# Performance work log

Hardware: AMD Instinct MI355X
Metric: run time of the kernel (lower is better)

## Reference

```python
import jax, jax.numpy as jnp
import numpy as np

NUM_HEADS = 8


def setup_inputs() -> dict:
    key = jax.random.key(0)
    ks = jax.random.split(key, 7)
    B, H, W, C = 1, 64, 64, 512
    x = jax.random.normal(ks[0], (B, H, W, C), dtype=jnp.float32)
    # lat in [-pi/2, pi/2), lon in [0, 2*pi) radians
    lat_grid = (jax.random.uniform(ks[1], (H, W), dtype=jnp.float32) - 0.5) * np.float32(np.pi)
    lon_grid = jax.random.uniform(ks[2], (H, W), dtype=jnp.float32) * np.float32(2 * np.pi)
    w_qkv = jax.random.normal(ks[3], (3 * C, C), dtype=jnp.float32) * 0.02
    b_qkv = jax.random.normal(ks[4], (3 * C,), dtype=jnp.float32) * 0.02
    w_out = jax.random.normal(ks[5], (C, C), dtype=jnp.float32) * 0.02
    b_out = jax.random.normal(ks[6], (C,), dtype=jnp.float32) * 0.02
    return {"x": x, "lat_grid": lat_grid, "lon_grid": lon_grid,
            "w_qkv": w_qkv, "b_qkv": b_qkv, "w_out": w_out, "b_out": b_out}


def _distance_bias(lat_grid, lon_grid):
    # Haversine great-circle distance between all pairs of grid points.
    lat = lat_grid.reshape(-1)  # [N]
    lon = lon_grid.reshape(-1)
    dlat = lat[None, :] - lat[:, None]  # [N, N]
    dlon = lon[None, :] - lon[:, None]
    a = jnp.sin(dlat / 2) ** 2 + jnp.cos(lat)[:, None] * jnp.cos(lat)[None, :] * jnp.sin(dlon / 2) ** 2
    dist = 2.0 * jnp.arcsin(jnp.sqrt(jnp.clip(a, 0.0, 1.0)))
    # torch .std() is unbiased (ddof=1)
    return -dist / jnp.std(dist, ddof=1)


def reference(x, lat_grid, lon_grid, w_qkv, b_qkv, w_out, b_out):
    B, H, W, C = x.shape
    nh = NUM_HEADS
    dh = C // nh
    N = H * W
    qkv = x @ w_qkv.T + b_qkv  # [B, H, W, 3C]
    qkv = qkv.reshape(B, N, 3, nh, dh)
    q = jnp.transpose(qkv[:, :, 0], (0, 2, 1, 3))  # [B, nh, N, dh]
    k = jnp.transpose(qkv[:, :, 1], (0, 2, 1, 3))
    v = jnp.transpose(qkv[:, :, 2], (0, 2, 1, 3))
    scale = np.float32(1.0 / np.sqrt(dh))
    attn = jnp.einsum("bhnd,bhmd->bhnm", q, k) * scale  # [B, nh, N, N]
    attn = attn + _distance_bias(lat_grid, lon_grid)[None, None]
    attn = jax.nn.softmax(attn, axis=-1)  # dropout is identity in eval
    out = jnp.einsum("bhnm,bhmd->bhnd", attn, v)  # [B, nh, N, dh]
    out = jnp.transpose(out, (0, 2, 1, 3)).reshape(B, H, W, C)
    return out @ w_out.T + b_out
```

## Files before the change

### kernel.cpp

```cpp
#include <hip/hip_runtime.h>
#include <hip/hip_bf16.h>


typedef __attribute__((ext_vector_type(8))) short bf16x8;
typedef __attribute__((ext_vector_type(4))) float f32x4;

#define MFMA16(a, b, c) __builtin_amdgcn_mfma_f32_16x16x32_bf16(a, b, c, 0, 0, 0)

__device__ __forceinline__ unsigned short f2b(float f) {
    union { float f; unsigned int i; } v;
    v.f = f;
    unsigned int lsb = (v.i >> 16) & 1u;
    unsigned int r = v.i + 0x7fffu + lsb;
    return (unsigned short)(r >> 16);
}

__global__ __launch_bounds__(256) void prep_kernel(
    const float* __restrict__ lat, const float* __restrict__ lon,
    float* __restrict__ dist, double* __restrict__ partials,
    const float* __restrict__ x, unsigned short* __restrict__ xb,
    const float* __restrict__ wq, unsigned short* __restrict__ wqb,
    const float* __restrict__ wo, unsigned short* __restrict__ wob) {
    __shared__ float sl_i[64], sc_i[64], so_i[64];
    __shared__ float sl_j[64], sc_j[64], so_j[64];
    __shared__ float dstage[64][65];
    __shared__ double rs[256], rs2[256];

    int b = blockIdx.x;
    int tid = threadIdx.x;

    if (b < 2080) {
        int ti = 0, rem = b;
        while (rem >= 64 - ti) { rem -= 64 - ti; ti++; }
        int tj = ti + rem;
        int i0 = ti << 6, j0 = tj << 6;

        if (tid < 64) {
            float la = lat[i0 + tid];
            sl_i[tid] = la; sc_i[tid] = __cosf(la); so_i[tid] = lon[i0 + tid];
        } else if (tid < 128) {
            int t = tid - 64;
            float la = lat[j0 + t];
            sl_j[t] = la; sc_j[t] = __cosf(la); so_j[t] = lon[j0 + t];
        }
        __syncthreads();

        float s = 0.f, s2 = 0.f;
        int col = tid & 63;
        int w = tid >> 6;
        int pcol = ((col & 15) << 2) + (col >> 4);
        float latj = sl_j[col], cj = sc_j[col], lonj = so_j[col];
#pragma unroll
        for (int kk = 0; kk < 16; kk++) {
            int row = (kk << 2) + w;
            float dlat = latj - sl_i[row];
            float dlon = lonj - so_i[row];
            float h1 = __sinf(0.5f * dlat);
            float h2 = __sinf(0.5f * dlon);
            float a = h1 * h1 + sc_i[row] * cj * h2 * h2;
            a = fminf(fmaxf(a, 0.0f), 1.0f);
            float d = 2.0f * asinf(sqrtf(a));
            dist[(size_t)(i0 + row) * 4096 + j0 + pcol] = d;
            dstage[row][col] = d;
            s += d;
            s2 += d * d;
        }
        if (ti != tj) {
            __syncthreads();
#pragma unroll
            for (int kk = 0; kk < 16; kk++) {
                int row2 = (kk << 2) + w;
                float dt = dstage[col][row2];
                dist[(size_t)(j0 + row2) * 4096 + i0 + pcol] = dt;
            }
            s *= 2.f; s2 *= 2.f;
        }
        rs[tid] = (double)s; rs2[tid] = (double)s2;
        __syncthreads();
        for (int off = 128; off > 0; off >>= 1) {
            if (tid < off) { rs[tid] += rs[tid + off]; rs2[tid] += rs2[tid + off]; }
            __syncthreads();
        }
        if (tid == 0) {
            partials[2 * b] = rs[0];
            partials[2 * b + 1] = rs2[0];
        }
        return;
    }

    const float* in; unsigned short* out; int t;
    if (b < 3104)      { in = x;  out = xb;  t = (b - 2080) * 256 + tid; }
    else if (b < 3488) { in = wq; out = wqb; t = (b - 3104) * 256 + tid; }
    else               { in = wo; out = wob; t = (b - 3488) * 256 + tid; }
    int l = t & 15, qd = (t >> 4) & 3, c = (t >> 6) & 15, g = t >> 10;
    const float* src = in + ((size_t)g * 16 + l) * 512 + c * 32 + qd * 8;
    float4 v0 = *(const float4*)src;
    float4 v1 = *(const float4*)(src + 4);
    ushort4 u0, u1;
    u0.x = f2b(v0.x); u0.y = f2b(v0.y); u0.z = f2b(v0.z); u0.w = f2b(v0.w);
    u1.x = f2b(v1.x); u1.y = f2b(v1.y); u1.z = f2b(v1.z); u1.w = f2b(v1.w);
    unsigned short* dst = out + (size_t)t * 8;
    *(ushort4*)dst = u0;
    *(ushort4*)(dst + 4) = u1;
}

__global__ __launch_bounds__(256) void qkv_gemm(
    const unsigned short* __restrict__ x, const unsigned short* __restrict__ w,
    const float* __restrict__ b,
    unsigned short* __restrict__ q, unsigned short* __restrict__ k,
    unsigned short* __restrict__ vt,
    const double* __restrict__ partials, float* __restrict__ neg_inv_std) {
    __shared__ unsigned short stage[64][72];
    __shared__ double rs[256], rs2[256];
    int lane = threadIdx.x & 63, wave = threadIdx.x >> 6;
    int l16 = lane & 15, quad = lane >> 4;

    if (blockIdx.x == 24) {
        if (blockIdx.y != 0) return;
        int tid = threadIdx.x;
        double s = 0.0, s2 = 0.0;
        for (int i = tid; i < 2080; i += 256) {
            s += partials[2 * i];
            s2 += partials[2 * i + 1];
        }
        rs[tid] = s; rs2[tid] = s2;
        __syncthreads();
        for (int off = 128; off > 0; off >>= 1) {
            if (tid < off) { rs[tid] += rs[tid + off]; rs2[tid] += rs2[tid + off]; }
            __syncthreads();
        }
        if (tid == 0) {
            double n = 16777216.0;
            double mean = rs[0] / n;
            double var = (rs2[0] - n * mean * mean) / (n - 1.0);
            *neg_inv_std = (float)(-1.0 / sqrt(var));
        }
        return;
    }

    int m0 = blockIdx.y * 64 + wave * 16;
    int n0 = blockIdx.x * 64;

    const unsigned short* abase = x + (size_t)(blockIdx.y * 4 + wave) * 8192 + lane * 8;
    f32x4 acc[4];
#pragma unroll
    for (int nb = 0; nb < 4; nb++) acc[nb] = (f32x4){0.f, 0.f, 0.f, 0.f};

    for (int k0 = 0; k0 < 512; k0 += 32) {
        bf16x8 af = *(const bf16x8*)(abase + (k0 >> 5) * 512);
#pragma unroll
        for (int nb = 0; nb < 4; nb++) {
            bf16x8 bf = *(const bf16x8*)(w + (size_t)((n0 >> 4) + nb) * 8192
                                           + (k0 >> 5) * 512 + lane * 8);
            acc[nb] = MFMA16(af, bf, acc[nb]);
        }
    }
    if (blockIdx.x < 8) {
#pragma unroll
        for (int nb = 0; nb < 4; nb++) {
            int j = n0 + nb * 16 + l16;
            float bj = b[j];
            int h = j >> 6, d = j & 63;
#pragma unroll
            for (int r = 0; r < 4; r++) {
                int n = m0 + quad * 4 + r;
                q[((size_t)h * 4096 + n) * 64 + d] = f2b((acc[nb][r] + bj) * 0.125f);
            }
        }
    } else if (blockIdx.x < 16) {
        int h = blockIdx.x - 8;
#pragma unroll
        for (int nb = 0; nb < 4; nb++) {
            int d = nb * 16 + l16;
            float bj = b[512 + h * 64 + d];
#pragma unroll
            for (int r = 0; r < 4; r++)
                stage[wave * 16 + quad * 4 + r][d] = f2b(acc[nb][r] + bj);
        }
        __syncthreads();
        unsigned short* kb = k + ((size_t)h << 18) + (size_t)blockIdx.y * 4096;
#pragma unroll
        for (int p = 0; p < 2; p++) {
            int rid = p * 256 + threadIdx.x;
            int t = rid >> 7;
            int rem = rid & 127;
            int half = rem >> 6, qd = (rem >> 4) & 3, l = rem & 15;
            const unsigned short* src = &stage[t * 16 + l][half * 32 + qd * 8];
            unsigned short* dst = kb + t * 1024 + half * 512 + qd * 128 + l * 8;
            *(uint4*)dst = *(const uint4*)src;
        }
    } else {
        int h = blockIdx.x - 16;
#pragma unroll
        for (int nb = 0; nb < 4; nb++) {
            int d = nb * 16 + l16;
            float bj = b[1024 + h * 64 + d];
#pragma unroll
            for (int r = 0; r < 4; r++)
                stage[d][quad * 16 + r * 4 + wave] = f2b(acc[nb][r] + bj);
        }
        __syncthreads();
        int t = threadIdx.x;
        int d = t >> 2;
        int nq = (t & 3) * 16;
        unsigned short* dst = vt + ((size_t)h << 18) + (size_t)blockIdx.y * 4096
                            + (d >> 4) * 1024 + ((nq >> 5) & 1) * 512
                            + ((nq >> 3) & 3) * 128 + (d & 15) * 8;
        const unsigned short* src = &stage[d][nq];
        *(uint4*)dst = *(const uint4*)src;
        *(uint4*)(dst + 128) = *(const uint4*)(src + 8);
    }
}

__device__ __forceinline__ void attn_step(
    const unsigned short* __restrict__ kptr, const unsigned short* __restrict__ vtp,
    short* __restrict__ pb, int h, int kv0, int lane, int l16, int quad,
    bf16x8 qf0, bf16x8 qf1, float4 (&dv)[4], const float* __restrict__ drow,
    int kv_next, float nis, f32x4 (&o)[4], float (&lam)[4]) {
    size_t tbase = ((size_t)h << 18) + ((size_t)kv0 << 6) + lane * 8;
    const unsigned short* kb = kptr + tbase;
    const unsigned short* vb = vtp + tbase;
    f32x4 s[4];
    __builtin_amdgcn_s_setprio(1);
#pragma unroll
    for (int cb = 0; cb < 4; cb++) {
        bf16x8 kf0 = *(const bf16x8*)(kb + cb * 1024);
        bf16x8 kf1 = *(const bf16x8*)(kb + cb * 1024 + 512);
        f32x4 z = (f32x4){0.f, 0.f, 0.f, 0.f};
        z = MFMA16(qf0, kf0, z);
        z = MFMA16(qf1, kf1, z);
        s[cb] = z;
    }
    __builtin_amdgcn_s_setprio(0);
    bf16x8 vf[8];
#pragma unroll
    for (int db = 0; db < 4; db++) {
        vf[2 * db]     = *(const bf16x8*)(vb + db * 1024);
        vf[2 * db + 1] = *(const bf16x8*)(vb + db * 1024 + 512);
    }
#pragma unroll
    for (int r = 0; r < 4; r++) {
        s[0][r] = fmaf(dv[r].x, nis, s[0][r]);
        s[1][r] = fmaf(dv[r].y, nis, s[1][r]);
        s[2][r] = fmaf(dv[r].z, nis, s[2][r]);
        s[3][r] = fmaf(dv[r].w, nis, s[3][r]);
    }
#pragma unroll
    for (int r = 0; r < 4; r++)
        dv[r] = *(const float4*)(drow + (size_t)r * 4096 + kv_next);
#pragma unroll
    for (int r = 0; r < 4; r++) {
        float p0 = __expf(s[0][r]);
        float p1 = __expf(s[1][r]);
        float p2 = __expf(s[2][r]);
        float p3 = __expf(s[3][r]);
        lam[r] += (p0 + p1) + (p2 + p3);
        unsigned int w0 = (unsigned int)f2b(p0) | ((unsigned int)f2b(p1) << 16);
        unsigned int w1 = (unsigned int)f2b(p2) | ((unsigned int)f2b(p3) << 16);
        uint2 pk; pk.x = w0; pk.y = w1;
        *(uint2*)(pb + (quad * 4 + r) * 72 + l16 * 4) = pk;
    }
    bf16x8 pf0 = *(const bf16x8*)(pb + l16 * 72 + quad * 8);
    bf16x8 pf1 = *(const bf16x8*)(pb + l16 * 72 + 32 + quad * 8);
    __builtin_amdgcn_s_setprio(1);
#pragma unroll
    for (int db = 0; db < 4; db++) {
        o[db] = MFMA16(pf0, vf[2 * db], o[db]);
        o[db] = MFMA16(pf1, vf[2 * db + 1], o[db]);
    }
    __builtin_amdgcn_s_setprio(0);
}

__global__ __launch_bounds__(512, 4) void attn_kernel(
    const unsigned short* __restrict__ q, const unsigned short* __restrict__ k,
    const unsigned short* __restrict__ vt, const float* __restrict__ dist,
    const float* __restrict__ nis_p, unsigned short* __restrict__ att) {
    __shared__ __align__(16) char smem[18432];
    int tid = threadIdx.x;
    int lane = tid & 63, wave = tid >> 6;
    int l16 = lane & 15, quad = lane >> 4;
    int b = blockIdx.x;
    int xcd = b & 7, j = b >> 3;
    int h  = (xcd & 3) * 2 + (j & 1);
    int qs = (xcd >> 2) * 64 + (j >> 1);
    int qgl = wave & 1;
    int qt = wave >> 1;
    int q0 = qs * 32 + qgl * 16;
    int kvbase = qt * 1024;
    float nis = *nis_p;

    short* pb = (short*)smem + wave * 1152;

    const unsigned short* qbase = q + ((size_t)h * 4096 + q0 + l16) * 64 + quad * 8;
    bf16x8 qf0 = *(const bf16x8*)(qbase);
    bf16x8 qf1 = *(const bf16x8*)(qbase + 32);

    f32x4 o[4];
    float lam[4];
#pragma unroll
    for (int r = 0; r < 4; r++) {
        lam[r] = 0.f;
        o[0][r] = 0.f; o[1][r] = 0.f; o[2][r] = 0.f; o[3][r] = 0.f;
    }

    const float* drow = dist + (size_t)(q0 + quad * 4) * 4096 + l16 * 4;
    float4 dv[4];
#pragma unroll
    for (int r = 0; r < 4; r++)
        dv[r] = *(const float4*)(drow + (size_t)r * 4096 + kvbase);

    for (int it = 0; it < 16; ++it) {
        int kv0 = kvbase + it * 64;
        int kvn = (it == 15) ? kvbase : kv0 + 64;
        attn_step(k, vt, pb, h, kv0, lane, l16, quad, qf0, qf1, dv, drow, kvn,
                  nis, o, lam);
    }

#pragma unroll
    for (int r = 0; r < 4; r++)
#pragma unroll
        for (int off = 1; off < 16; off <<= 1)
            lam[r] += __shfl_xor(lam[r], off, 64);

    __syncthreads();
    float* obuf = (float*)smem;
    float* lbuf = (float*)(smem + 8192);
    if (l16 == 0)
#pragma unroll
        for (int r = 0; r < 4; r++)
            lbuf[qt * 32 + qgl * 16 + quad * 4 + r] = lam[r];
    if (qt == 0) {
#pragma unroll
        for (int db = 0; db < 4; db++)
#pragma unroll
            for (int r = 0; r < 4; r++)
                obuf[(qgl * 16 + quad * 4 + r) * 64 + db * 16 + l16] = o[db][r];
    }
    __syncthreads();
    if (qt == 1) {
#pragma unroll
        for (int db = 0; db < 4; db++)
#pragma unroll
            for (int r = 0; r < 4; r++)
                obuf[(qgl * 16 + quad * 4 + r) * 64 + db * 16 + l16] += o[db][r];
    }
    __syncthreads();
    if (qt == 2) {
#pragma unroll
        for (int db = 0; db < 4; db++)
#pragma unroll
            for (int r = 0; r < 4; r++)
                obuf[(qgl * 16 + quad * 4 + r) * 64 + db * 16 + l16] += o[db][r];
    }
    __syncthreads();
    if (qt == 3) {
#pragma unroll
        for (int db = 0; db < 4; db++)
#pragma unroll
            for (int r = 0; r < 4; r++)
                obuf[(qgl * 16 + quad * 4 + r) * 64 + db * 16 + l16] += o[db][r];
    }
    __syncthreads();

    int rl = tid >> 4;
    int d4 = (tid & 15) * 4;
    float L = lbuf[rl] + lbuf[32 + rl] + lbuf[64 + rl] + lbuf[96 + rl];
    float rinv = 1.0f / L;
    const float* ob = obuf + rl * 64 + d4;
    ushort4 ua;
    ua.x = f2b(ob[0] * rinv); ua.y = f2b(ob[1] * rinv);
    ua.z = f2b(ob[2] * rinv); ua.w = f2b(ob[3] * rinv);
    int row = qs * 32 + rl;
    int col = h * 64 + d4;
    size_t dst = (size_t)(row >> 4) * 8192 + (col >> 5) * 512
               + ((col >> 3) & 3) * 128 + (row & 15) * 8 + (col & 7);
    *(ushort4*)(att + dst) = ua;
}

__global__ __launch_bounds__(256) void out_gemm(
    const unsigned short* __restrict__ att, const unsigned short* __restrict__ w,
    const float* __restrict__ b, float* __restrict__ out) {
    int lane = threadIdx.x & 63, wave = threadIdx.x >> 6;
    int l16 = lane & 15, quad = lane >> 4;
    int m0 = blockIdx.y * 64 + wave * 16;
    int n0 = blockIdx.x * 64;

    const unsigned short* abase = att + (size_t)(blockIdx.y * 4 + wave) * 8192 + lane * 8;
    f32x4 acc[4];
#pragma unroll
    for (int nb = 0; nb < 4; nb++) acc[nb] = (f32x4){0.f, 0.f, 0.f, 0.f};

    for (int k0 = 0; k0 < 512; k0 += 32) {
        bf16x8 af = *(const bf16x8*)(abase + (k0 >> 5) * 512);
#pragma unroll
        for (int nb = 0; nb < 4; nb++) {
            bf16x8 bf = *(const bf16x8*)(w + (size_t)((n0 >> 4) + nb) * 8192
                                           + (k0 >> 5) * 512 + lane * 8);
            acc[nb] = MFMA16(af, bf, acc[nb]);
        }
    }
#pragma unroll
    for (int nb = 0; nb < 4; nb++) {
        float bj = b[n0 + nb * 16 + l16];
#pragma unroll
        for (int r = 0; r < 4; r++)
            out[(size_t)(m0 + quad * 4 + r) * 512 + n0 + nb * 16 + l16] =
                acc[nb][r] + bj;
    }
}

extern "C" void kernel_launch(void* const* d_in, const int* in_sizes, int n_in,
                              void* d_out, int out_size, void* d_ws, size_t ws_size,
                              hipStream_t stream) {
    const float* x    = (const float*)d_in[0];
    const float* lat  = (const float*)d_in[1];
    const float* lon  = (const float*)d_in[2];
    const float* wqkv = (const float*)d_in[3];
    const float* bqkv = (const float*)d_in[4];
    const float* wout = (const float*)d_in[5];
    const float* bout = (const float*)d_in[6];
    float* out = (float*)d_out;

    char* ws = (char*)d_ws;
    float* dist        = (float*)ws;
    double* partials   = (double*)(ws + 67108864);
    float* nis         = (float*)(ws + 67108864 + 65536);
    unsigned short* q  = (unsigned short*)(ws + 67108864 + 65600);
    unsigned short* k  = q  + (size_t)8 * 4096 * 64;
    unsigned short* vt = k  + (size_t)8 * 4096 * 64;
    unsigned short* att = vt + (size_t)8 * 4096 * 64;
    unsigned short* xb  = att + (size_t)4096 * 512;
    unsigned short* wqb = xb  + (size_t)4096 * 512;
    unsigned short* wob = wqb + (size_t)1536 * 512;

    prep_kernel<<<3616, 256, 0, stream>>>(lat, lon, dist, partials,
                                          x, xb, wqkv, wqb, wout, wob);
    qkv_gemm<<<dim3(25, 64), 256, 0, stream>>>(xb, wqb, bqkv, q, k, vt,
                                               partials, nis);
    attn_kernel<<<1024, 512, 0, stream>>>(q, k, vt, dist, nis, att);
    out_gemm<<<dim3(8, 64), 256, 0, stream>>>(att, wob, bout, out);
}
```

Measured before the change: 212.9 us.

## Software-pipeline attention loop by computing next tile's QK scores early

```diff
diff --git a/kernel.cpp b/kernel.cpp
--- a/kernel.cpp
+++ b/kernel.cpp
@@ -210,65 +210,6 @@
         *(uint4*)dst = *(const uint4*)src;
         *(uint4*)(dst + 128) = *(const uint4*)(src + 8);
     }
-}
-
-__device__ __forceinline__ void attn_step(
-    const unsigned short* __restrict__ kptr, const unsigned short* __restrict__ vtp,
-    short* __restrict__ pb, int h, int kv0, int lane, int l16, int quad,
-    bf16x8 qf0, bf16x8 qf1, float4 (&dv)[4], const float* __restrict__ drow,
-    int kv_next, float nis, f32x4 (&o)[4], float (&lam)[4]) {
-    size_t tbase = ((size_t)h << 18) + ((size_t)kv0 << 6) + lane * 8;
-    const unsigned short* kb = kptr + tbase;
-    const unsigned short* vb = vtp + tbase;
-    f32x4 s[4];
-    __builtin_amdgcn_s_setprio(1);
-#pragma unroll
-    for (int cb = 0; cb < 4; cb++) {
-        bf16x8 kf0 = *(const bf16x8*)(kb + cb * 1024);
-        bf16x8 kf1 = *(const bf16x8*)(kb + cb * 1024 + 512);
-        f32x4 z = (f32x4){0.f, 0.f, 0.f, 0.f};
-        z = MFMA16(qf0, kf0, z);
-        z = MFMA16(qf1, kf1, z);
-        s[cb] = z;
-    }
-    __builtin_amdgcn_s_setprio(0);
-    bf16x8 vf[8];
-#pragma unroll
-    for (int db = 0; db < 4; db++) {
-        vf[2 * db]     = *(const bf16x8*)(vb + db * 1024);
-        vf[2 * db + 1] = *(const bf16x8*)(vb + db * 1024 + 512);
-    }
-#pragma unroll
-    for (int r = 0; r < 4; r++) {
-        s[0][r] = fmaf(dv[r].x, nis, s[0][r]);
-        s[1][r] = fmaf(dv[r].y, nis, s[1][r]);
-        s[2][r] = fmaf(dv[r].z, nis, s[2][r]);
-        s[3][r] = fmaf(dv[r].w, nis, s[3][r]);
-    }
-#pragma unroll
-    for (int r = 0; r < 4; r++)
-        dv[r] = *(const float4*)(drow + (size_t)r * 4096 + kv_next);
-#pragma unroll
-    for (int r = 0; r < 4; r++) {
-        float p0 = __expf(s[0][r]);
-        float p1 = __expf(s[1][r]);
-        float p2 = __expf(s[2][r]);
-        float p3 = __expf(s[3][r]);
-        lam[r] += (p0 + p1) + (p2 + p3);
-        unsigned int w0 = (unsigned int)f2b(p0) | ((unsigned int)f2b(p1) << 16);
-        unsigned int w1 = (unsigned int)f2b(p2) | ((unsigned int)f2b(p3) << 16);
-        uint2 pk; pk.x = w0; pk.y = w1;
-        *(uint2*)(pb + (quad * 4 + r) * 72 + l16 * 4) = pk;
-    }
-    bf16x8 pf0 = *(const bf16x8*)(pb + l16 * 72 + quad * 8);
-    bf16x8 pf1 = *(const bf16x8*)(pb + l16 * 72 + 32 + quad * 8);
-    __builtin_amdgcn_s_setprio(1);
-#pragma unroll
-    for (int db = 0; db < 4; db++) {
-        o[db] = MFMA16(pf0, vf[2 * db], o[db]);
-        o[db] = MFMA16(pf1, vf[2 * db + 1], o[db]);
-    }
-    __builtin_amdgcn_s_setprio(0);
 }
 
 __global__ __launch_bounds__(512, 4) void attn_kernel(
@@ -295,6 +236,8 @@
     bf16x8 qf0 = *(const bf16x8*)(qbase);
     bf16x8 qf1 = *(const bf16x8*)(qbase + 32);
 
+    size_t hbase = ((size_t)h << 18) + (size_t)lane * 8;
+
     f32x4 o[4];
     float lam[4];
 #pragma unroll
@@ -309,11 +252,80 @@
     for (int r = 0; r < 4; r++)
         dv[r] = *(const float4*)(drow + (size_t)r * 4096 + kvbase);
 
+    f32x4 s[4];
+    {
+        const unsigned short* kb = k + hbase + ((size_t)kvbase << 6);
+        __builtin_amdgcn_s_setprio(1);
+#pragma unroll
+        for (int cb = 0; cb < 4; cb++) {
+            bf16x8 kf0 = *(const bf16x8*)(kb + cb * 1024);
+            bf16x8 kf1 = *(const bf16x8*)(kb + cb * 1024 + 512);
+            f32x4 z = (f32x4){0.f, 0.f, 0.f, 0.f};
+            z = MFMA16(qf0, kf0, z);
+            z = MFMA16(qf1, kf1, z);
+            s[cb] = z;
+        }
+        __builtin_amdgcn_s_setprio(0);
+    }
+
     for (int it = 0; it < 16; ++it) {
         int kv0 = kvbase + it * 64;
         int kvn = (it == 15) ? kvbase : kv0 + 64;
-        attn_step(k, vt, pb, h, kv0, lane, l16, quad, qf0, qf1, dv, drow, kvn,
-                  nis, o, lam);
+#pragma unroll
+        for (int r = 0; r < 4; r++) {
+            s[0][r] = fmaf(dv[r].x, nis, s[0][r]);
+            s[1][r] = fmaf(dv[r].y, nis, s[1][r]);
+            s[2][r] = fmaf(dv[r].z, nis, s[2][r]);
+            s[3][r] = fmaf(dv[r].w, nis, s[3][r]);
+        }
+#pragma unroll
+        for (int r = 0; r < 4; r++)
+            dv[r] = *(const float4*)(drow + (size_t)r * 4096 + kvn);
+#pragma unroll
+        for (int r = 0; r < 4; r++) {
+            float p0 = __expf(s[0][r]);
+            float p1 = __expf(s[1][r]);
+            float p2 = __expf(s[2][r]);
+            float p3 = __expf(s[3][r]);
+            lam[r] += (p0 + p1) + (p2 + p3);
+            unsigned int w0 = (unsigned int)f2b(p0) | ((unsigned int)f2b(p1) << 16);
+            unsigned int w1 = (unsigned int)f2b(p2) | ((unsigned int)f2b(p3) << 16);
+            uint2 pk; pk.x = w0; pk.y = w1;
+            *(uint2*)(pb + (quad * 4 + r) * 72 + l16 * 4) = pk;
+        }
+        const unsigned short* vb = vt + hbase + ((size_t)kv0 << 6);
+        bf16x8 vf[8];
+#pragma unroll
+        for (int db = 0; db < 4; db++) {
+            vf[2 * db]     = *(const bf16x8*)(vb + db * 1024);
+            vf[2 * db + 1] = *(const bf16x8*)(vb + db * 1024 + 512);
+        }
+        f32x4 sn[4];
+        {
+            const unsigned short* kb = k + hbase + ((size_t)kvn << 6);
+            __builtin_amdgcn_s_setprio(1);
+#pragma unroll
+            for (int cb = 0; cb < 4; cb++) {
+                bf16x8 kf0 = *(const bf16x8*)(kb + cb * 1024);
+                bf16x8 kf1 = *(const bf16x8*)(kb + cb * 1024 + 512);
+                f32x4 z = (f32x4){0.f, 0.f, 0.f, 0.f};
+                z = MFMA16(qf0, kf0, z);
+                z = MFMA16(qf1, kf1, z);
+                sn[cb] = z;
+            }
+            __builtin_amdgcn_s_setprio(0);
+        }
+        bf16x8 pf0 = *(const bf16x8*)(pb + l16 * 72 + quad * 8);
+        bf16x8 pf1 = *(const bf16x8*)(pb + l16 * 72 + 32 + quad * 8);
+        __builtin_amdgcn_s_setprio(1);
+#pragma unroll
+        for (int db = 0; db < 4; db++) {
+            o[db] = MFMA16(pf0, vf[2 * db], o[db]);
+            o[db] = MFMA16(pf1, vf[2 * db + 1], o[db]);
+        }
+        __builtin_amdgcn_s_setprio(0);
+#pragma unroll
+        for (int cb = 0; cb < 4; cb++) s[cb] = sn[cb];
     }
 
 #pragma unroll
```

Result: no change. 215.8 us (+1.3%).
